# Kernel tuning notes

Hardware: AMD Instinct MI355X
Metric: run time of the kernel (lower is better)

Reference implementation:

```python
import jax, jax.numpy as jnp
import numpy as np

EPS = 1e-5

def _conv(x, w, pad):
    return jax.lax.conv_general_dilated(
        x, w, window_strides=(1, 1), padding=((pad, pad), (pad, pad)),
        dimension_numbers=('NCHW', 'OIHW', 'NCHW'))

def _dyn_branch(x, w, d):
    # x: [N,C,H,W]; w: [N,9,H,W] softmax weights; d: dilation.
    # Equivalent to unfold(k=3, dilation=d, padding=d) + bmm with w,
    # done as 9 shifted zero-padded slices (row-major kernel order).
    N, C, H, W = x.shape
    xp = jnp.pad(x, ((0, 0), (0, 0), (d, d), (d, d)))
    out = jnp.zeros_like(x)
    k = 0
    for dy in (-d, 0, d):
        for dx in (-d, 0, d):
            patch = xp[:, :, d + dy:d + dy + H, d + dx:d + dx + W]
            out = out + patch * w[:, k:k + 1]
            k += 1
    return out

def setup_inputs() -> dict:
    key = jax.random.key(0)
    k1, k2, k3 = jax.random.split(key, 3)
    C = 256
    x = jax.random.normal(k1, (2, C, 96, 96), dtype=jnp.float32)
    W_cat = jax.random.normal(k2, (45, C, 3, 3), dtype=jnp.float32) * 0.05
    W_scale = jax.random.normal(k3, (C, 6 * C, 1, 1), dtype=jnp.float32) * 0.05
    gamma = jnp.ones((C,), dtype=jnp.float32)
    beta = jnp.zeros((C,), dtype=jnp.float32)
    return {"x": x, "W_cat": W_cat, "W_scale": W_scale, "gamma": gamma, "beta": beta}

def reference(x, W_cat, W_scale, gamma, beta):
    guidance = _conv(x, W_cat, pad=1)  # [N,45,H,W]
    outs = [x]
    for i, d in enumerate((1, 6, 12, 24, 36)):
        w = jax.nn.softmax(guidance[:, 9 * i:9 * (i + 1)], axis=1)  # [N,9,H,W]
        outs.append(_dyn_branch(x, w, d))
    cat = jnp.concatenate(outs, axis=1)  # [N, 6C, H, W]
    y = _conv(cat, W_scale, pad=0)       # [N, C, H, W]
    # BatchNorm2d in training mode (batch statistics, biased variance)
    mean = jnp.mean(y, axis=(0, 2, 3), keepdims=True)
    var = jnp.var(y, axis=(0, 2, 3), keepdims=True)
    y = (y - mean) * jax.lax.rsqrt(var + EPS)
    return y * gamma[None, :, None, None] + beta[None, :, None, None]
```

## Files before the change

kernel.cpp:

```cpp
#include <hip/hip_runtime.h>

typedef __bf16 bf16x8 __attribute__((ext_vector_type(8)));
typedef float f32x4 __attribute__((ext_vector_type(4)));

#define HW 9216
#define ZSLAB 9216
#define XTILE 32768
#define GUARDL 55296

__device__ __forceinline__ unsigned short f2bf(float f) {
  unsigned u = __float_as_uint(f);
  unsigned r = (u + 0x7FFFu + ((u >> 16) & 1u)) >> 16;
  return (unsigned short)r;
}
__device__ __forceinline__ float bf2f(unsigned short h) {
  return __uint_as_float(((unsigned)h) << 16);
}

__device__ __forceinline__ void async16(const unsigned short* g, unsigned short* l) {
  __builtin_amdgcn_global_load_lds(
      (const __attribute__((address_space(1))) unsigned int*)g,
      (__attribute__((address_space(3))) unsigned int*)l, 16, 0, 0);
}

template <int O>
__device__ __forceinline__ void tapfma(float* y, uint4 lo, uint4 hi, uint4 wv) {
  const unsigned short* lu = (const unsigned short*)&lo;
  const unsigned short* hu = (const unsigned short*)&hi;
  const unsigned short* wu = (const unsigned short*)&wv;
#pragma unroll
  for (int j = 0; j < 8; ++j) {
    unsigned short zz = (O + j < 8) ? lu[O + j] : hu[O + j - 8];
    y[j] += bf2f(wu[j]) * bf2f(zz);
  }
}

__device__ __forceinline__ uint4 lload(const unsigned short* lz, bool v, int idx) {
  return *(const uint4*)(lz + (v ? idx : GUARDL));
}

template <int B, int D>
__device__ __forceinline__ void branchL(float* y, const unsigned short* lz,
                                        const unsigned short* __restrict__ gb,
                                        int h, int w0) {
  const int sbase = B * 9216;
  const bool cmv = ((unsigned)(w0 - ((D == 1 || D == 6) ? 8 : (D == 12 ? 16 : (D == 24 ? 24 : 40)))) <= 88u);
  const bool cm2v = ((unsigned)(w0 - ((D == 12) ? 8 : 32)) <= 88u);
  const bool cpv = ((unsigned)(w0 + ((D == 1 || D == 6) ? 8 : (D == 12 ? 16 : (D == 24 ? 24 : 40)))) <= 88u);
  const bool cp2v = ((unsigned)(w0 + ((D == 12) ? 8 : 32)) <= 88u);

#pragma unroll
  for (int r = 0; r < 3; ++r) {
    int hh = h + (r - 1) * D;
    bool rv = ((unsigned)hh < 96u);
    int rb = sbase + hh * 96;
    const int K0 = (B - 1) * 9 + r * 3;
    uint4 wv0 = *(const uint4*)(gb + (size_t)((K0 + 0) * 2) * HW);
    uint4 wv1 = *(const uint4*)(gb + (size_t)((K0 + 1) * 2) * HW);
    uint4 wv2 = *(const uint4*)(gb + (size_t)((K0 + 2) * 2) * HW);
    if constexpr (D == 1 || D == 6) {
      uint4 Wm = lload(lz, rv && cmv, rb + w0 - 8);
      uint4 W0 = lload(lz, rv, rb + w0);
      uint4 Wp = lload(lz, rv && cpv, rb + w0 + 8);
      if constexpr (D == 1) {
        tapfma<7>(y, Wm, W0, wv0);
        tapfma<0>(y, W0, W0, wv1);
        tapfma<1>(y, W0, Wp, wv2);
      } else {
        tapfma<2>(y, Wm, W0, wv0);
        tapfma<0>(y, W0, W0, wv1);
        tapfma<6>(y, W0, Wp, wv2);
      }
    } else if constexpr (D == 24) {
      uint4 Wm = lload(lz, rv && cmv, rb + w0 - 24);
      uint4 W0 = lload(lz, rv, rb + w0);
      uint4 Wp = lload(lz, rv && cpv, rb + w0 + 24);
      tapfma<0>(y, Wm, Wm, wv0);
      tapfma<0>(y, W0, W0, wv1);
      tapfma<0>(y, Wp, Wp, wv2);
    } else {
      constexpr int co = (D == 12) ? 16 : 40;
      constexpr int ci = (D == 12) ? 8 : 32;
      uint4 Wa = lload(lz, rv && cmv, rb + w0 - co);
      uint4 Wb = lload(lz, rv && cm2v, rb + w0 - ci);
      uint4 W0 = lload(lz, rv, rb + w0);
      uint4 Wc = lload(lz, rv && cp2v, rb + w0 + ci);
      uint4 Wd = lload(lz, rv && cpv, rb + w0 + co);
      tapfma<4>(y, Wa, Wb, wv0);
      tapfma<0>(y, W0, W0, wv1);
      tapfma<4>(y, Wc, Wd, wv2);
    }
  }
}

__global__ __launch_bounds__(256) void init_all(const float* __restrict__ x,
                                                const float* __restrict__ Ws,
                                                const float* __restrict__ Wc,
                                                unsigned short* __restrict__ xb,
                                                unsigned short* __restrict__ Wsb,
                                                unsigned short* __restrict__ Wcb) {
  __shared__ float tile[64][65];
  int id = blockIdx.x;
  int t = threadIdx.x;
  if (id < 1152) {
    int bx = id % 144, by = (id / 144) % 4, n = id / 576;
    int p0 = bx * 64, ci0 = by * 64;
    int cl = t & 63, q = t >> 6;
#pragma unroll
    for (int i = 0; i < 16; ++i) {
      int cir = q + i * 4;
      tile[cir][cl] = x[((size_t)(n * 256 + ci0 + cir)) * HW + p0 + cl];
    }
    __syncthreads();
    int R = n * HW + p0 + cl;
    int Rt = R >> 7, Rl = R & 127;
#pragma unroll
    for (int i = 0; i < 2; ++i) {
      int cloc = q * 2 + i;
      unsigned rr[4];
#pragma unroll
      for (int jj = 0; jj < 4; ++jj) {
        unsigned short a = f2bf(tile[cloc * 8 + jj * 2][cl]);
        unsigned short b = f2bf(tile[cloc * 8 + jj * 2 + 1][cl]);
        rr[jj] = (unsigned)a | ((unsigned)b << 16);
      }
      *(uint4*)(xb + (size_t)Rt * XTILE + (by * 8 + cloc) * 1024 + Rl * 8) =
          make_uint4(rr[0], rr[1], rr[2], rr[3]);
    }
  } else {
    int u = (id - 1152) * 256 + t;
    if (u < 393216) {
      int r = u >> 8, k = u & 255;
      Wsb[(size_t)(r >> 7) * XTILE + (k >> 3) * 1024 + (r & 127) * 8 + (k & 7)] =
          f2bf(Ws[(size_t)(r & 255) * 1536 + (r >> 8) * 256 + k]);
    } else {
      int v = u - 393216;
      if (v < 110592) {
        int co = v / 2304, rr = v % 2304;
        int j = rr >> 8, ci = rr & 255;
        Wcb[v] = (co < 45) ? f2bf(Wc[(size_t)co * 2304 + ci * 9 + j]) : (unsigned short)0;
      }
    }
  }
}

__global__ __launch_bounds__(256) void gemms(const unsigned short* __restrict__ xb,
                                             const unsigned short* __restrict__ Wsb,
                                             const unsigned short* __restrict__ Wcb,
                                             unsigned short* __restrict__ z,
                                             unsigned short* __restrict__ gsmb) {
  __shared__ unsigned short smem[16384];
  int id = blockIdx.x;
  int t = threadIdx.x;
  int wid = t >> 6, lane = t & 63;
  int q = lane >> 4, ln = lane & 15;

  if (id < 288) {
    unsigned short* As = smem;
    unsigned short* Bs = smem + 4096;
    int m0 = id * 64;
    int mm = t >> 2, kq = t & 3;
    int m = m0 + mm;
    int img = m / HW, p = m % HW;
    int h = p / 96, w = p % 96;
    int mbase = img * HW;
    int nn = t >> 2;
    f32x4 acc[3] = {};
    uint4 aA0, aA1, aB0, aB1;

    {
      int hh = h - 1, ww = w - 1;
      bool valid = ((unsigned)hh < 96u) & ((unsigned)ww < 96u);
      int R = mbase + hh * 96 + ww;
      const unsigned short* pa =
          xb + (long)(R >> 7) * XTILE + kq * 1024 + (R & 127) * 8;
      aA0 = valid ? *(const uint4*)pa : make_uint4(0, 0, 0, 0);
      aA1 = valid ? *(const uint4*)(pa + 4096) : make_uint4(0, 0, 0, 0);
      if (t < 192) {
        const unsigned short* pb = Wcb + (size_t)nn * 2304 + kq * 8;
        aB0 = *(const uint4*)pb;
        aB1 = *(const uint4*)(pb + 32);
      }
    }

    for (int s = 0; s < 36; ++s) {
      ((uint4*)As)[kq * 64 + mm] = aA0;
      ((uint4*)As)[(kq + 4) * 64 + mm] = aA1;
      if (t < 192) {
        ((uint4*)Bs)[kq * 48 + nn] = aB0;
        ((uint4*)Bs)[(kq + 4) * 48 + nn] = aB1;
      }
      __syncthreads();
      if (s + 1 < 36) {
        int s1 = s + 1;
        int j = s1 >> 2;
        int hh = h + j / 3 - 1, ww = w + j % 3 - 1;
        bool valid = ((unsigned)hh < 96u) & ((unsigned)ww < 96u);
        int R = mbase + hh * 96 + ww;
        const unsigned short* pa = xb + (long)(R >> 7) * XTILE +
                                   ((s1 & 3) * 8 + kq) * 1024 + (R & 127) * 8;
        aA0 = valid ? *(const uint4*)pa : make_uint4(0, 0, 0, 0);
        aA1 = valid ? *(const uint4*)(pa + 4096) : make_uint4(0, 0, 0, 0);
        if (t < 192) {
          const unsigned short* pb = Wcb + (size_t)nn * 2304 + s1 * 64 + kq * 8;
          aB0 = *(const uint4*)pb;
          aB1 = *(const uint4*)(pb + 32);
        }
      }
#pragma unroll
      for (int kk = 0; kk < 2; ++kk) {
        bf16x8 a = ((const bf16x8*)As)[(kk * 4 + q) * 64 + wid * 16 + ln];
#pragma unroll
        for (int fn = 0; fn < 3; ++fn) {
          bf16x8 b = ((const bf16x8*)Bs)[(kk * 4 + q) * 48 + fn * 16 + ln];
          acc[fn] = __builtin_amdgcn_mfma_f32_16x16x32_bf16(a, b, acc[fn], 0, 0, 0);
        }
      }
      __syncthreads();
    }

    float* LDSf = (float*)smem;
#pragma unroll
    for (int fn = 0; fn < 3; ++fn)
#pragma unroll
      for (int r = 0; r < 4; ++r)
        LDSf[(wid * 16 + q * 4 + r) * 49 + fn * 16 + ln] = acc[fn][r];
    __syncthreads();
    if (t < 64) {
      const float* row = LDSf + t * 49;
      int mg = m0 + t;
      int img2 = mg / HW, p2 = mg - img2 * HW;
      for (int grp = 0; grp < 5; ++grp) {
        float v[9], mx = -1e30f;
#pragma unroll
        for (int k = 0; k < 9; ++k) { v[k] = row[grp * 9 + k]; mx = fmaxf(mx, v[k]); }
        float sum = 0.f;
#pragma unroll
        for (int k = 0; k < 9; ++k) { v[k] = __expf(v[k] - mx); sum += v[k]; }
        float inv = 1.f / sum;
#pragma unroll
        for (int k = 0; k < 9; ++k) {
          int col = grp * 9 + k;
          gsmb[((size_t)(col * 2 + img2)) * HW + p2] = f2bf(v[k] * inv);
        }
      }
    }
  } else {
    int zid = id - 288;
    int mt = zid % 144, ct = zid / 144;
    int m0 = mt * 128, c0 = ct * 128;
    int wm = (wid >> 1) * 64, wn = (wid & 1) * 64;
    bool isB = wid >= 2;
    const unsigned short* gsrc =
        (isB ? Wsb + (size_t)ct * XTILE : xb + (size_t)mt * XTILE) + lane * 8;
    unsigned short* lb = smem + (isB ? 8192 : 0);
    int ow = (wid & 1) * 4;
    f32x4 acc[4][4] = {};

#pragma unroll
    for (int kq = 0; kq < 4; ++kq)
      async16(gsrc + (ow + kq) * 512, lb + (ow + kq) * 512);
    __syncthreads();

    for (int s = 0; s < 8; ++s) {
      int cur = s & 1, nxt = cur ^ 1;
      if (s < 7) {
#pragma unroll
        for (int kq = 0; kq < 4; ++kq)
          async16(gsrc + (s + 1) * 4096 + (ow + kq) * 512,
                  lb + nxt * 4096 + (ow + kq) * 512);
      }
      const unsigned short* Asc = smem + cur * 4096;
      const unsigned short* Bsc = smem + 8192 + cur * 4096;
      bf16x8 a[4], b[4];
#pragma unroll
      for (int f = 0; f < 4; ++f) {
        a[f] = ((const bf16x8*)Asc)[q * 128 + wm + f * 16 + ln];
        b[f] = ((const bf16x8*)Bsc)[q * 128 + wn + f * 16 + ln];
      }
#pragma unroll
      for (int fm = 0; fm < 4; ++fm)
#pragma unroll
        for (int fn = 0; fn < 4; ++fn)
          acc[fm][fn] = __builtin_amdgcn_mfma_f32_16x16x32_bf16(a[fm], b[fn], acc[fm][fn], 0, 0, 0);
      __syncthreads();
    }

    int sl = c0 >> 8, cb = c0 & 255;
    int img = m0 / HW;
    int pbase = m0 - img * HW;
#pragma unroll
    for (int fm = 0; fm < 4; ++fm) {
      int p = pbase + wm + fm * 16 + q * 4;
#pragma unroll
      for (int fn = 0; fn < 4; ++fn) {
        int ch = cb + wn + fn * 16 + ln;
        size_t slab = ((size_t)(sl * 256 + ch) * 2 + img) * ZSLAB;
        unsigned lo = (unsigned)f2bf(acc[fm][fn][0]) | ((unsigned)f2bf(acc[fm][fn][1]) << 16);
        unsigned hi = (unsigned)f2bf(acc[fm][fn][2]) | ((unsigned)f2bf(acc[fm][fn][3]) << 16);
        *(uint2*)(z + slab + p) = make_uint2(lo, hi);
      }
    }
  }
}

__global__ __launch_bounds__(576, 1) void accum_chw(const unsigned short* __restrict__ z,
                                                    const unsigned short* __restrict__ gsmb,
                                                    float* __restrict__ yacc,
                                                    float* __restrict__ stats) {
  extern __shared__ unsigned short lz[];
  int bid = blockIdx.x;
  int img = bid & 1, ch = bid >> 1;
  int t = threadIdx.x;
  int wv_id = t >> 6, lane = t & 63;

#pragma unroll
  for (int i = 0; i < 12; ++i) {
    int op = wv_id + i * 9;
    int s = op / 18;
    int off = (op - s * 18) * 512;
    async16(z + ((size_t)((s * 256 + ch) * 2 + img)) * ZSLAB + off + lane * 8,
            lz + s * 9216 + off);
  }
  if (t == 0) *(uint4*)(lz + GUARDL) = make_uint4(0u, 0u, 0u, 0u);
  __syncthreads();

  float s1 = 0.f, s2 = 0.f;
#pragma unroll
  for (int rep = 0; rep < 2; ++rep) {
    int c = t + rep * 576;
    int h = c / 12;
    int w0 = (c - h * 12) * 8;
    int p0 = h * 96 + w0;
    const unsigned short* gb = gsmb + (size_t)img * HW + p0;

    float y[8];
    {
      uint4 v = *(const uint4*)(lz + p0);
      const unsigned short* u = (const unsigned short*)&v;
#pragma unroll
      for (int j = 0; j < 8; ++j) y[j] = bf2f(u[j]);
    }
    branchL<1, 1>(y, lz, gb, h, w0);
    branchL<2, 6>(y, lz, gb, h, w0);
    branchL<3, 12>(y, lz, gb, h, w0);
    branchL<4, 24>(y, lz, gb, h, w0);
    branchL<5, 36>(y, lz, gb, h, w0);

    size_t ybase = ((size_t)(img * 256 + ch)) * HW + p0;
    *(float4*)(yacc + ybase) = make_float4(y[0], y[1], y[2], y[3]);
    *(float4*)(yacc + ybase + 4) = make_float4(y[4], y[5], y[6], y[7]);

#pragma unroll
    for (int j = 0; j < 8; ++j) { s1 += y[j]; s2 += y[j] * y[j]; }
  }

#pragma unroll
  for (int off = 1; off <= 32; off <<= 1) {
    s1 += __shfl_xor(s1, off);
    s2 += __shfl_xor(s2, off);
  }
  if (lane == 0) {
    atomicAdd(&stats[ch], s1);
    atomicAdd(&stats[256 + ch], s2);
  }
}

__global__ __launch_bounds__(256) void bn_apply(const float* __restrict__ yacc,
                                                const float* __restrict__ stats,
                                                const float* __restrict__ gamma,
                                                const float* __restrict__ beta,
                                                float* __restrict__ out) {
  int q = blockIdx.x * 256 + threadIdx.x;
  int ch = (q / 2304) & 255;
  const float inv_cnt = 1.f / 18432.f;
  float mean = stats[ch] * inv_cnt;
  float var = stats[256 + ch] * inv_cnt - mean * mean;
  float sc = rsqrtf(var + 1e-5f) * gamma[ch];
  float sh = beta[ch] - mean * sc;
  float4 v = *(const float4*)(yacc + (size_t)q * 4);
  float4 o = make_float4(v.x * sc + sh, v.y * sc + sh, v.z * sc + sh, v.w * sc + sh);
  *(float4*)(out + (size_t)q * 4) = o;
}

extern "C" void kernel_launch(void* const* d_in, const int* in_sizes, int n_in,
                              void* d_out, int out_size, void* d_ws, size_t ws_size,
                              hipStream_t stream) {
  const float* x = (const float*)d_in[0];
  const float* Wc = (const float*)d_in[1];
  const float* Ws = (const float*)d_in[2];
  const float* gamma = (const float*)d_in[3];
  const float* beta = (const float*)d_in[4];
  float* out = (float*)d_out;

  unsigned short* xb = (unsigned short*)d_ws;
  unsigned short* Wsb = xb + 4718592;
  unsigned short* Wcb = Wsb + 393216;
  unsigned short* gsmb = Wcb + 110592;
  unsigned short* z = gsmb + 829440;
  float* yacc = (float*)(z + 28311552);
  float* stats = yacc + 4718592;

  hipMemsetAsync(stats, 0, 512 * sizeof(float), stream);
  init_all<<<3120, 256, 0, stream>>>(x, Ws, Wc, xb, Wsb, Wcb);
  gemms<<<2016, 256, 0, stream>>>(xb, Wsb, Wcb, z, gsmb);
  accum_chw<<<512, 576, 110624, stream>>>(z, gsmb, yacc, stats);
  bn_apply<<<4608, 256, 0, stream>>>(yacc, stats, gamma, beta, out);
}
```

Measured before the change: 173.5 us.

## Double-buffer accum_chw slabs in LDS and shrink block to raise occupancy

The accumulation kernel used to load all six bf16 slabs (about 110 KB of LDS) before computing, which allowed only one 576-thread block per CU. It now keeps two 9216-element LDS buffers and streams one slab per branch, prefetching the next slab while the current branch computes. The identity slab is read straight from global memory, and each of 384 threads handles three pixel groups. LDS use drops to about 37 KB so several blocks can share a CU, at the cost of five extra barriers and more registers per thread.

```diff
diff --git a/kernel.cpp b/kernel.cpp
--- a/kernel.cpp
+++ b/kernel.cpp
@@ -6,7 +6,7 @@
 #define HW 9216
 #define ZSLAB 9216
 #define XTILE 32768
-#define GUARDL 55296
+#define GUARDL 18432
 
 __device__ __forceinline__ unsigned short f2bf(float f) {
   unsigned u = __float_as_uint(f);
@@ -40,10 +40,9 @@
 }
 
 template <int B, int D>
-__device__ __forceinline__ void branchL(float* y, const unsigned short* lz,
+__device__ __forceinline__ void branchP(float* y, const unsigned short* lz, int sbase,
                                         const unsigned short* __restrict__ gb,
                                         int h, int w0) {
-  const int sbase = B * 9216;
   const bool cmv = ((unsigned)(w0 - ((D == 1 || D == 6) ? 8 : (D == 12 ? 16 : (D == 24 ? 24 : 40)))) <= 88u);
   const bool cm2v = ((unsigned)(w0 - ((D == 12) ? 8 : 32)) <= 88u);
   const bool cpv = ((unsigned)(w0 + ((D == 1 || D == 6) ? 8 : (D == 12 ? 16 : (D == 24 ? 24 : 40)))) <= 88u);
@@ -93,6 +92,16 @@
   }
 }
 
+template <int B, int D>
+__device__ __forceinline__ void branch3(float* y0, float* y1, float* y2,
+                                        const unsigned short* lz, int sbase,
+                                        const unsigned short* __restrict__ gsi,
+                                        int t) {
+  { const int c = t;       int h = c / 12, w0 = (c - h * 12) * 8; branchP<B, D>(y0, lz, sbase, gsi + h * 96 + w0, h, w0); }
+  { const int c = t + 384; int h = c / 12, w0 = (c - h * 12) * 8; branchP<B, D>(y1, lz, sbase, gsi + h * 96 + w0, h, w0); }
+  { const int c = t + 768; int h = c / 12, w0 = (c - h * 12) * 8; branchP<B, D>(y2, lz, sbase, gsi + h * 96 + w0, h, w0); }
+}
+
 __global__ __launch_bounds__(256) void init_all(const float* __restrict__ x,
                                                 const float* __restrict__ Ws,
                                                 const float* __restrict__ Wc,
@@ -304,55 +313,94 @@
   }
 }
 
-__global__ __launch_bounds__(576, 1) void accum_chw(const unsigned short* __restrict__ z,
-                                                    const unsigned short* __restrict__ gsmb,
-                                                    float* __restrict__ yacc,
-                                                    float* __restrict__ stats) {
+__global__ __launch_bounds__(384) void accum_chw(const unsigned short* __restrict__ z,
+                                                 const unsigned short* __restrict__ gsmb,
+                                                 float* __restrict__ yacc,
+                                                 float* __restrict__ stats) {
   extern __shared__ unsigned short lz[];
   int bid = blockIdx.x;
   int img = bid & 1, ch = bid >> 1;
   int t = threadIdx.x;
   int wv_id = t >> 6, lane = t & 63;
-
-#pragma unroll
-  for (int i = 0; i < 12; ++i) {
-    int op = wv_id + i * 9;
-    int s = op / 18;
-    int off = (op - s * 18) * 512;
-    async16(z + ((size_t)((s * 256 + ch) * 2 + img)) * ZSLAB + off + lane * 8,
-            lz + s * 9216 + off);
-  }
+  const size_t zsl = (size_t)(ch * 2 + img) * ZSLAB;
+
+#define STG(SLAB, BUF)                                                        \
+  {                                                                           \
+    _Pragma("unroll") for (int i = 0; i < 3; ++i) {                           \
+      int off = (wv_id + i * 6) * 512;                                        \
+      async16(z + zsl + (size_t)((SLAB)*512) * ZSLAB + off + lane * 8,        \
+              lz + (BUF) + off + lane * 8);                                   \
+    }                                                                         \
+  }
+
+  STG(1, 0);
   if (t == 0) *(uint4*)(lz + GUARDL) = make_uint4(0u, 0u, 0u, 0u);
+
+  const unsigned short* gsi = gsmb + (size_t)img * HW;
+  float y0[8], y1[8], y2[8];
+  {
+    const int c = t; int h = c / 12, w0 = (c - h * 12) * 8;
+    uint4 v = *(const uint4*)(z + zsl + h * 96 + w0);
+    const unsigned short* u = (const unsigned short*)&v;
+#pragma unroll
+    for (int j = 0; j < 8; ++j) y0[j] = bf2f(u[j]);
+  }
+  {
+    const int c = t + 384; int h = c / 12, w0 = (c - h * 12) * 8;
+    uint4 v = *(const uint4*)(z + zsl + h * 96 + w0);
+    const unsigned short* u = (const unsigned short*)&v;
+#pragma unroll
+    for (int j = 0; j < 8; ++j) y1[j] = bf2f(u[j]);
+  }
+  {
+    const int c = t + 768; int h = c / 12, w0 = (c - h * 12) * 8;
+    uint4 v = *(const uint4*)(z + zsl + h * 96 + w0);
+    const unsigned short* u = (const unsigned short*)&v;
+#pragma unroll
+    for (int j = 0; j < 8; ++j) y2[j] = bf2f(u[j]);
+  }
+
   __syncthreads();
+  STG(2, 9216);
+  branch3<1, 1>(y0, y1, y2, lz, 0, gsi, t);
+  __syncthreads();
+  STG(3, 0);
+  branch3<2, 6>(y0, y1, y2, lz, 9216, gsi, t);
+  __syncthreads();
+  STG(4, 9216);
+  branch3<3, 12>(y0, y1, y2, lz, 0, gsi, t);
+  __syncthreads();
+  STG(5, 0);
+  branch3<4, 24>(y0, y1, y2, lz, 9216, gsi, t);
+  __syncthreads();
+  branch3<5, 36>(y0, y1, y2, lz, 0, gsi, t);
+#undef STG
 
   float s1 = 0.f, s2 = 0.f;
-#pragma unroll
-  for (int rep = 0; rep < 2; ++rep) {
-    int c = t + rep * 576;
-    int h = c / 12;
-    int w0 = (c - h * 12) * 8;
-    int p0 = h * 96 + w0;
-    const unsigned short* gb = gsmb + (size_t)img * HW + p0;
-
-    float y[8];
-    {
-      uint4 v = *(const uint4*)(lz + p0);
-      const unsigned short* u = (const unsigned short*)&v;
-#pragma unroll
-      for (int j = 0; j < 8; ++j) y[j] = bf2f(u[j]);
-    }
-    branchL<1, 1>(y, lz, gb, h, w0);
-    branchL<2, 6>(y, lz, gb, h, w0);
-    branchL<3, 12>(y, lz, gb, h, w0);
-    branchL<4, 24>(y, lz, gb, h, w0);
-    branchL<5, 36>(y, lz, gb, h, w0);
-
-    size_t ybase = ((size_t)(img * 256 + ch)) * HW + p0;
-    *(float4*)(yacc + ybase) = make_float4(y[0], y[1], y[2], y[3]);
-    *(float4*)(yacc + ybase + 4) = make_float4(y[4], y[5], y[6], y[7]);
-
-#pragma unroll
-    for (int j = 0; j < 8; ++j) { s1 += y[j]; s2 += y[j] * y[j]; }
+  const size_t ybq = (size_t)(img * 256 + ch) * HW;
+  {
+    const int c = t; int h = c / 12, w0 = (c - h * 12) * 8;
+    size_t yb = ybq + h * 96 + w0;
+    *(float4*)(yacc + yb) = make_float4(y0[0], y0[1], y0[2], y0[3]);
+    *(float4*)(yacc + yb + 4) = make_float4(y0[4], y0[5], y0[6], y0[7]);
+#pragma unroll
+    for (int j = 0; j < 8; ++j) { s1 += y0[j]; s2 += y0[j] * y0[j]; }
+  }
+  {
+    const int c = t + 384; int h = c / 12, w0 = (c - h * 12) * 8;
+    size_t yb = ybq + h * 96 + w0;
+    *(float4*)(yacc + yb) = make_float4(y1[0], y1[1], y1[2], y1[3]);
+    *(float4*)(yacc + yb + 4) = make_float4(y1[4], y1[5], y1[6], y1[7]);
+#pragma unroll
+    for (int j = 0; j < 8; ++j) { s1 += y1[j]; s2 += y1[j] * y1[j]; }
+  }
+  {
+    const int c = t + 768; int h = c / 12, w0 = (c - h * 12) * 8;
+    size_t yb = ybq + h * 96 + w0;
+    *(float4*)(yacc + yb) = make_float4(y2[0], y2[1], y2[2], y2[3]);
+    *(float4*)(yacc + yb + 4) = make_float4(y2[4], y2[5], y2[6], y2[7]);
+#pragma unroll
+    for (int j = 0; j < 8; ++j) { s1 += y2[j]; s2 += y2[j] * y2[j]; }
   }
 
 #pragma unroll
@@ -404,6 +452,6 @@
   hipMemsetAsync(stats, 0, 512 * sizeof(float), stream);
   init_all<<<3120, 256, 0, stream>>>(x, Ws, Wc, xb, Wsb, Wcb);
   gemms<<<2016, 256, 0, stream>>>(xb, Wsb, Wcb, z, gsmb);
-  accum_chw<<<512, 576, 110624, stream>>>(z, gsmb, yacc, stats);
+  accum_chw<<<512, 384, 36896, stream>>>(z, gsmb, yacc, stats);
   bn_apply<<<4608, 256, 0, stream>>>(yacc, stats, gamma, beta, out);
 }
```

Measured after the change: 570.5 us. 3.29x slower.
